# Kernel tuning notes

Hardware: AMD Instinct MI355X
Metric: run time of the kernel (lower is better)

Reference implementation:

```python
import jax, jax.numpy as jnp
import numpy as np

# dims: L blocks, S cur_seq, M memory_len, B batch, D embed, H heads, IN input_dim
L, S, M, B, D, H, IN = 4, 512, 512, 8, 1024, 16, 128
HD = D // H
GRU_BIAS = 2.0  # config['gru_bias']


def _ln(x, s, b, eps=1e-5):
    mu = x.mean(-1, keepdims=True)
    var = ((x - mu) ** 2).mean(-1, keepdims=True)
    return (x - mu) * jax.lax.rsqrt(var + eps) * s + b


def _pos_emb(full_seq, dim):
    # SinusoidalPE: freqs = arange(0, dim, 2.0); inv = 10000**(-freqs/dim); seq descending
    freqs = jnp.arange(0, dim, 2.0)
    inv = 10000.0 ** (-freqs / dim)
    seq = jnp.arange(full_seq - 1, -1, -1.0)
    ang = seq[:, None] * inv[None, :]
    return jnp.concatenate([jnp.sin(ang), jnp.cos(ang)], axis=-1)  # (F, dim)


def _rel_shift(x):
    # x: (q, k, b, h) -> Transformer-XL relative shift
    q, k, b, h = x.shape
    xp = jnp.pad(x, ((0, 0), (1, 0), (0, 0), (0, 0)))
    return xp.reshape(k + 1, q, b, h)[1:].reshape(q, k, b, h)


def _gru(x, y, Wr, Ur, Wz, Uz, Wg, Ug):
    r = jax.nn.sigmoid(y @ Wr + x @ Ur)
    z = jax.nn.sigmoid(y @ Wz + x @ Uz - GRU_BIAS)
    hcand = jnp.tanh(y @ Wg + (r * x) @ Ug)
    return (1.0 - z) * x + z * hcand


def setup_inputs() -> dict:
    key = jax.random.key(0)
    ks = iter(jax.random.split(key, 64))

    def mat(*shape):
        return jax.random.normal(next(ks), shape, jnp.float32) * (shape[-2] ** -0.5)

    return dict(
        h=jax.random.normal(next(ks), (B, S, IN), jnp.float32),
        memory=jnp.zeros((L, M, B, D), jnp.float32),
        We=mat(IN, D), be=jnp.zeros((D,), jnp.float32),
        ln1_s=jnp.ones((L, D), jnp.float32), ln1_b=jnp.zeros((L, D), jnp.float32),
        ln2_s=jnp.ones((L, D), jnp.float32), ln2_b=jnp.zeros((L, D), jnp.float32),
        Wq=mat(L, D, D), bq=jnp.zeros((L, D), jnp.float32),
        Wk=mat(L, D, D), bk=jnp.zeros((L, D), jnp.float32),
        Wv=mat(L, D, D), bv=jnp.zeros((L, D), jnp.float32),
        Wr=mat(L, D, D), br=jnp.zeros((L, D), jnp.float32),
        Wo=mat(L, D, D), bo=jnp.zeros((L, D), jnp.float32),
        u=jax.random.normal(next(ks), (L, H, HD), jnp.float32) * 0.02,
        vb=jax.random.normal(next(ks), (L, H, HD), jnp.float32) * 0.02,
        gWr=mat(L, 2, D, D), gUr=mat(L, 2, D, D),
        gWz=mat(L, 2, D, D), gUz=mat(L, 2, D, D),
        gWg=mat(L, 2, D, D), gUg=mat(L, 2, D, D),
        fW1=mat(L, D, 4 * D), fb1=jnp.zeros((L, 4 * D), jnp.float32),
        fW2=mat(L, 4 * D, D), fb2=jnp.zeros((L, D), jnp.float32),
    )


def reference(h, memory, We, be, ln1_s, ln1_b, ln2_s, ln2_b,
              Wq, bq, Wk, bk, Wv, bv, Wr, br, Wo, bo, u, vb,
              gWr, gUr, gWz, gUz, gWg, gUg, fW1, fb1, fW2, fb2):
    x = jnp.transpose(h, (1, 0, 2))                      # (S, B, IN)
    x = jax.nn.gelu(x @ We + be, approximate=False)      # (S, B, D)
    F = S + M
    pos = _pos_emb(F, D)                                 # (F, D)
    mask = jnp.triu(jnp.ones((S, F), bool), k=1 + M)     # (S, F)
    scale = HD ** -0.5
    out = x
    for i in range(L):
        full = jnp.concatenate([memory[i], out], axis=0)  # (F, B, D)
        qn = _ln(out, ln1_s[i], ln1_b[i])
        kn = _ln(full, ln1_s[i], ln1_b[i])
        q = (qn @ Wq[i] + bq[i]).reshape(S, B, H, HD)
        k = (kn @ Wk[i] + bk[i]).reshape(F, B, H, HD)
        v = (kn @ Wv[i] + bv[i]).reshape(F, B, H, HD)
        r = (pos @ Wr[i] + br[i]).reshape(F, H, HD)
        content = jnp.einsum('ibhd,jbhd->ijbh', q + u[i], k)
        position = _rel_shift(jnp.einsum('ibhd,jhd->ijbh', q + vb[i], r))
        attn = (content + position) * scale               # (S, F, B, H)
        attn = jnp.where(mask[:, :, None, None], -1e30, attn)
        a = jax.nn.softmax(attn, axis=1)
        y = jnp.einsum('ijbh,jbhd->ibhd', a, v).reshape(S, B, D) @ Wo[i] + bo[i]
        y = jax.nn.gelu(y, approximate=False)
        out1 = _gru(out, y, gWr[i, 0], gUr[i, 0], gWz[i, 0], gUz[i, 0], gWg[i, 0], gUg[i, 0])
        e = _ln(out1, ln2_s[i], ln2_b[i])
        e = jax.nn.gelu(e @ fW1[i] + fb1[i], approximate=False)
        e = jax.nn.gelu(e @ fW2[i] + fb2[i], approximate=False)
        out = _gru(out1, e, gWr[i, 1], gUr[i, 1], gWz[i, 1], gUz[i, 1], gWg[i, 1], gUg[i, 1])
    return jnp.transpose(out, (1, 0, 2))                  # (B, S, D)
```

## Files before the change

kernel.cpp:

```cpp
#include <hip/hip_runtime.h>

typedef unsigned short u16;
typedef unsigned long long u64;
typedef __attribute__((ext_vector_type(8))) short bf16x8;
typedef __attribute__((ext_vector_type(4))) float f32x4;

#define DEVI __device__ __forceinline__

DEVI u16 f2b(float f) {
  unsigned u = __float_as_uint(f);
  u += 0x7fffu + ((u >> 16) & 1u);
  return (u16)(u >> 16);
}
DEVI float b2f(u16 v) { return __uint_as_float((unsigned)v << 16); }
DEVI float gelu_f(float x) { return 0.5f * x * (1.f + erff(x * 0.70710678118654752f)); }
DEVI float sigm_f(float x) { return 1.f / (1.f + expf(-x)); }

DEVI void gload16(const void* g, void* l) {
  __builtin_amdgcn_global_load_lds((__attribute__((address_space(1))) void*)g,
                                   (__attribute__((address_space(3))) void*)l, 16, 0, 0);
}

__global__ __launch_bounds__(256) void gemm_bt(
    const u16* __restrict__ A, const u16* __restrict__ Bt,
    const float* __restrict__ bias, float* __restrict__ C32, u16* __restrict__ C16,
    int M, int N, int K, int ldA, int ldB, int ldC,
    long long sA, long long sBb, long long sBh, long long sC, int nH, int flags)
{
  __shared__ __align__(16) u16 Sm[2][256 * 64];
  const int z = blockIdx.z;
  const int zb = z / nH, zh = z - zb * nH;
  A  += (long long)z * sA;
  Bt += (long long)zb * sBb + (long long)zh * sBh;
  const long long cOff = (long long)z * sC;
  const int m0 = blockIdx.x * 128, n0 = blockIdx.y * 128;
  const int t = threadIdx.x, lane = t & 63;
  const int wm = ((t >> 7) & 1) * 64, wn = ((t >> 6) & 1) * 64;

  f32x4 acc[4][4];
#pragma unroll
  for (int i = 0; i < 4; ++i)
#pragma unroll
    for (int j = 0; j < 4; ++j) { f32x4 zz = {0.f, 0.f, 0.f, 0.f}; acc[i][j] = zz; }

  auto stage = [&](int buf, int k0) {
#pragma unroll
    for (int r = 0; r < 4; ++r) {
      const int c = r * 256 + t;
      const int row = c >> 3;
      const int col = (c & 7) << 3;
      int ga = m0 + row; if (ga >= M) ga = M - 1;
      gload16(A + (long long)ga * ldA + (k0 + col),
              &Sm[buf][(size_t)(r * 256 + (t & 192)) * 8]);
      int gb = n0 + row; if (gb >= N) gb = N - 1;
      gload16(Bt + (long long)gb * ldB + (k0 + col),
              &Sm[buf][(size_t)(1024 + r * 256 + (t & 192)) * 8]);
    }
  };

  auto compute = [&](int buf) {
    const u16* As = &Sm[buf][0];
    const u16* Bs = &Sm[buf][128 * 64];
#pragma unroll
    for (int ks = 0; ks < 2; ++ks) {
      const int ko = ks * 32 + ((lane >> 4) << 3);
      bf16x8 af[4], bfv[4];
#pragma unroll
      for (int i = 0; i < 4; ++i)
        af[i] = *(const bf16x8*)&As[(wm + i * 16 + (lane & 15)) * 64 + ko];
#pragma unroll
      for (int i = 0; i < 4; ++i)
        bfv[i] = *(const bf16x8*)&Bs[(wn + i * 16 + (lane & 15)) * 64 + ko];
#pragma unroll
      for (int mi = 0; mi < 4; ++mi)
#pragma unroll
        for (int ni = 0; ni < 4; ++ni)
          acc[mi][ni] = __builtin_amdgcn_mfma_f32_16x16x32_bf16(af[mi], bfv[ni], acc[mi][ni], 0, 0, 0);
    }
  };

  stage(0, 0);
  __syncthreads();
  int cur = 0;
  for (int k0 = 64; k0 < K; k0 += 64) {
    stage(cur ^ 1, k0);
    compute(cur);
    __syncthreads();
    cur ^= 1;
  }
  compute(cur);

  const int cb = n0 + wn + (lane & 15);
  const int rb = m0 + wm + ((lane >> 4) << 2);
#pragma unroll
  for (int ni = 0; ni < 4; ++ni) {
    const int col = cb + ni * 16;
    if (col >= N) continue;
    const float bv = (flags & 2) ? bias[col] : 0.f;
#pragma unroll
    for (int mi = 0; mi < 4; ++mi) {
#pragma unroll
      for (int q = 0; q < 4; ++q) {
        const int row = rb + mi * 16 + q;
        if (row >= M) continue;
        float x = acc[mi][ni][q] + bv;
        if (flags & 1) x = gelu_f(x);
        const long long o = cOff + (long long)row * ldC + col;
        if (flags & 4) C32[o] = x;
        if (flags & 8) C16[o] = f2b(x);
      }
    }
  }
}

__global__ __launch_bounds__(256) void fused_attn(
    const u16* __restrict__ Qb,
    const u16* __restrict__ Kb,
    const u16* __restrict__ Vt,
    const u16* __restrict__ Rh,
    const float* __restrict__ uK,
    const float* __restrict__ vbR,
    u16* __restrict__ Y)
{
  constexpr int F = 1024;
  const int i0 = blockIdx.x * 64;
  const int bh = blockIdx.y;
  const int h = bh & 15;

  __shared__ __align__(16) u16 Qs[64 * 64];
  __shared__ __align__(16) u16 Ks[64 * 64];
  __shared__ __align__(16) u16 Vs[64 * 64];
  __shared__ __align__(16) u16 Rs[2][64 * 64];
  __shared__ u16 PBs[64][132];
  __shared__ __align__(16) u16 Ps[4][16][72];
  __shared__ float uKs[64];
  __shared__ float vbRs[2][64];

  const int t = threadIdx.x;
  const int lane = t & 63;
  const int wq = t >> 6;
  const int l15 = lane & 15, lhi = lane >> 4;

  const u16* Qg = Qb + ((size_t)bh * 512 + i0) * 64;
  const u16* Kg = Kb + (size_t)bh * F * 64;
  const u16* Vg = Vt + (size_t)bh * 64 * F;
  const u16* Rg = Rh + (size_t)h * F * 64;
  const float* uKg = uK + (size_t)bh * F;
  const float* vbRg = vbR + (size_t)h * F;

  auto stageQ = [&]() {
#pragma unroll
    for (int rnd = 0; rnd < 2; ++rnd) {
      const int idx = rnd * 256 + t;
      const int row = idx >> 3;
      const int gs = (idx & 7) ^ (row & 7);
      gload16(Qg + row * 64 + gs * 8, Qs + (size_t)(rnd * 256 + (t & 192)) * 8);
    }
  };
  auto stageK = [&](int j0) {
#pragma unroll
    for (int rnd = 0; rnd < 2; ++rnd) {
      const int idx = rnd * 256 + t;
      const int row = idx >> 3;
      const int gs = (idx & 7) ^ (row & 7);
      gload16(Kg + (j0 + row) * 64 + gs * 8, Ks + (size_t)(rnd * 256 + (t & 192)) * 8);
    }
  };
  auto stageV = [&](int j0) {
#pragma unroll
    for (int rnd = 0; rnd < 2; ++rnd) {
      const int idx = rnd * 256 + t;
      const int row = idx >> 3;
      const int gs = (idx & 7) ^ (row & 7);
      gload16(Vg + row * F + j0 + gs * 8, Vs + (size_t)(rnd * 256 + (t & 192)) * 8);
    }
  };
  auto stageR = [&](u16* dst, int cbase) {
#pragma unroll
    for (int rnd = 0; rnd < 2; ++rnd) {
      const int idx = rnd * 256 + t;
      const int row = idx >> 3;
      const int gs = (idx & 7) ^ (row & 7);
      int grow = cbase + row; if (grow > 1023) grow = 1023;
      gload16(Rg + grow * 64 + gs * 8, dst + (size_t)(rnd * 256 + (t & 192)) * 8);
    }
  };

  stageQ();
  const int c_lo0 = 448 - i0;
  stageR(Rs[0], c_lo0);
  if (t < 64) {
    int c = c_lo0 + t; if (c > 1023) c = 1023;
    vbRs[0][t] = vbRg[c];
  }

  f32x4 Oacc[4];
#pragma unroll
  for (int i = 0; i < 4; ++i) { f32x4 zz = {0.f, 0.f, 0.f, 0.f}; Oacc[i] = zz; }
  float mrow[4] = {-3.0e38f, -3.0e38f, -3.0e38f, -3.0e38f};
  float lrow[4] = {0.f, 0.f, 0.f, 0.f};

  const int nT = i0 / 64 + 9;
  for (int st = 0; st < nT; ++st) {
    const int j0 = st * 64;
    const int c_hi = j0 - i0 + 512;
    __syncthreads();
    stageK(j0);
    stageV(j0);
    stageR(Rs[(st + 1) & 1], c_hi);
    if (t < 64) uKs[t] = uKg[j0 + t];
    else if (t < 128) {
      int c = c_hi + (t - 64); if (c > 1023) c = 1023;
      vbRs[(st + 1) & 1][t - 64] = vbRg[c];
    }
    __syncthreads();

    const u16* RsLo = Rs[st & 1];
    const u16* RsHi = Rs[(st + 1) & 1];
    const float* vLo = vbRs[st & 1];
    const float* vHi = vbRs[(st + 1) & 1];

    f32x4 cacc[4], pbacc[8];
#pragma unroll
    for (int i = 0; i < 4; ++i) { f32x4 zz = {0.f, 0.f, 0.f, 0.f}; cacc[i] = zz; }
#pragma unroll
    for (int i = 0; i < 8; ++i) { f32x4 zz = {0.f, 0.f, 0.f, 0.f}; pbacc[i] = zz; }
#pragma unroll
    for (int ks = 0; ks < 2; ++ks) {
      const int arow = wq * 16 + l15;
      const bf16x8 a = *(const bf16x8*)&Qs[arow * 64 + (((ks * 4 + lhi) ^ (arow & 7)) << 3)];
#pragma unroll
      for (int ni = 0; ni < 4; ++ni) {
        const int brow = ni * 16 + l15;
        const bf16x8 bk_ = *(const bf16x8*)&Ks[brow * 64 + (((ks * 4 + lhi) ^ (brow & 7)) << 3)];
        cacc[ni] = __builtin_amdgcn_mfma_f32_16x16x32_bf16(a, bk_, cacc[ni], 0, 0, 0);
      }
#pragma unroll
      for (int ni = 0; ni < 8; ++ni) {
        const int brow = (ni & 3) * 16 + l15;
        const u16* rt = (ni < 4) ? RsLo : RsHi;
        const bf16x8 br_ = *(const bf16x8*)&rt[brow * 64 + (((ks * 4 + lhi) ^ (brow & 7)) << 3)];
        pbacc[ni] = __builtin_amdgcn_mfma_f32_16x16x32_bf16(a, br_, pbacc[ni], 0, 0, 0);
      }
    }
#pragma unroll
    for (int ni = 0; ni < 8; ++ni)
#pragma unroll
      for (int qq = 0; qq < 4; ++qq)
        PBs[wq * 16 + lhi * 4 + qq][ni * 16 + l15] = f2b(pbacc[ni][qq]);

    const int lim = i0 - j0 + 512;
    float sc[4][4];
#pragma unroll
    for (int ni = 0; ni < 4; ++ni) {
      const int dj = ni * 16 + l15;
      const float uk = uKs[dj];
#pragma unroll
      for (int qq = 0; qq < 4; ++qq) {
        const int di = wq * 16 + lhi * 4 + qq;
        const int cc = dj - di + 63;
        const float pb = b2f(PBs[di][cc]);
        const float vr = (cc < 64) ? vLo[cc] : vHi[cc - 64];
        float s = (cacc[ni][qq] + uk + pb + vr) * 0.125f;
        if (dj - di > lim) s = -1e30f;
        sc[ni][qq] = s;
      }
    }

    float nm[4], esc[4];
#pragma unroll
    for (int qq = 0; qq < 4; ++qq) {
      float r = fmaxf(fmaxf(sc[0][qq], sc[1][qq]), fmaxf(sc[2][qq], sc[3][qq]));
      r = fmaxf(r, __shfl_xor(r, 1));
      r = fmaxf(r, __shfl_xor(r, 2));
      r = fmaxf(r, __shfl_xor(r, 4));
      r = fmaxf(r, __shfl_xor(r, 8));
      nm[qq] = fmaxf(mrow[qq], r);
      esc[qq] = expf(mrow[qq] - nm[qq]);
      mrow[qq] = nm[qq];
    }
    float ps[4][4];
    float rsum[4] = {0.f, 0.f, 0.f, 0.f};
#pragma unroll
    for (int ni = 0; ni < 4; ++ni)
#pragma unroll
      for (int qq = 0; qq < 4; ++qq) {
        float p = expf(sc[ni][qq] - nm[qq]);
        ps[ni][qq] = p;
        rsum[qq] += p;
      }
#pragma unroll
    for (int qq = 0; qq < 4; ++qq) {
      float r = rsum[qq];
      r += __shfl_xor(r, 1);
      r += __shfl_xor(r, 2);
      r += __shfl_xor(r, 4);
      r += __shfl_xor(r, 8);
      lrow[qq] = lrow[qq] * esc[qq] + r;
    }
#pragma unroll
    for (int nd = 0; nd < 4; ++nd)
#pragma unroll
      for (int qq = 0; qq < 4; ++qq) Oacc[nd][qq] *= esc[qq];

#pragma unroll
    for (int ni = 0; ni < 4; ++ni)
#pragma unroll
      for (int qq = 0; qq < 4; ++qq)
        Ps[wq][lhi * 4 + qq][ni * 16 + l15] = f2b(ps[ni][qq]);
#pragma unroll
    for (int ks = 0; ks < 2; ++ks) {
      const bf16x8 pa = *(const bf16x8*)&Ps[wq][l15][ks * 32 + lhi * 8];
#pragma unroll
      for (int nd = 0; nd < 4; ++nd) {
        const int vrow = nd * 16 + l15;
        const bf16x8 vb_ = *(const bf16x8*)&Vs[vrow * 64 + (((ks * 4 + lhi) ^ (vrow & 7)) << 3)];
        Oacc[nd] = __builtin_amdgcn_mfma_f32_16x16x32_bf16(pa, vb_, Oacc[nd], 0, 0, 0);
      }
    }
  }

  float inv[4];
#pragma unroll
  for (int qq = 0; qq < 4; ++qq) inv[qq] = 1.f / lrow[qq];
  const int b = bh >> 4;
#pragma unroll
  for (int nd = 0; nd < 4; ++nd)
#pragma unroll
    for (int qq = 0; qq < 4; ++qq) {
      const int row = i0 + wq * 16 + lhi * 4 + qq;
      const int d = nd * 16 + l15;
      Y[(size_t)row * 8192 + b * 1024 + h * 64 + d] = f2b(Oacc[nd][qq] * inv[qq]);
    }
}

__global__ __launch_bounds__(256) void uk_kernel(const u16* __restrict__ Kb,
                                                 const float* __restrict__ u,
                                                 float* __restrict__ uK)
{
  const long long idx = (long long)blockIdx.x * 256 + threadIdx.x;
  const int h = (int)((idx >> 10) & 15);
  const u16* k = Kb + idx * 64;
  const float* uh = u + h * 64;
  float s = 0.f;
#pragma unroll
  for (int j = 0; j < 8; ++j) {
    bf16x8 kv = *(const bf16x8*)&k[j * 8];
#pragma unroll
    for (int e = 0; e < 8; ++e) s += b2f((u16)kv[e]) * uh[j * 8 + e];
  }
  uK[idx] = s;
}

__global__ __launch_bounds__(256) void vbr_kernel(const u16* __restrict__ Rh,
                                                  const float* __restrict__ vb,
                                                  float* __restrict__ vbR)
{
  const long long idx = (long long)blockIdx.x * 256 + threadIdx.x;
  const int h = (int)(idx >> 10);
  const u16* r = Rh + idx * 64;
  const float* vh = vb + h * 64;
  float s = 0.f;
#pragma unroll
  for (int j = 0; j < 8; ++j) {
    bf16x8 rv = *(const bf16x8*)&r[j * 8];
#pragma unroll
    for (int e = 0; e < 8; ++e) s += b2f((u16)rv[e]) * vh[j * 8 + e];
  }
  vbR[idx] = s;
}

#define MAXW 20
struct WPack {
  const float* src[MAXW];
  u16* dst[MAXW];
  int K[MAXW], N[MAXW];
  int tilePrefix[MAXW + 1];
  int nm;
};

__global__ __launch_bounds__(256) void wtrans_kernel(WPack p) {
  int bid = blockIdx.x;
  int m = 0;
  while (m < p.nm && bid >= p.tilePrefix[m + 1]) ++m;
  if (m >= p.nm) return;
  const int lt = bid - p.tilePrefix[m];
  const int K = p.K[m], N = p.N[m];
  const int tN = N >> 5;
  const int kt = lt / tN, nt = lt - kt * tN;
  const int k0 = kt << 5, n0 = nt << 5;
  const float* src = p.src[m];
  u16* dst = p.dst[m];
  __shared__ float tile[32][33];
  const int t = threadIdx.x;
  const int r = t >> 3, c4 = (t & 7) << 2;
  float4 v = *(const float4*)&src[(size_t)(k0 + r) * N + n0 + c4];
  tile[r][c4 + 0] = v.x; tile[r][c4 + 1] = v.y; tile[r][c4 + 2] = v.z; tile[r][c4 + 3] = v.w;
  __syncthreads();
  u16 o0 = f2b(tile[c4 + 0][r]);
  u16 o1 = f2b(tile[c4 + 1][r]);
  u16 o2 = f2b(tile[c4 + 2][r]);
  u16 o3 = f2b(tile[c4 + 3][r]);
  u64 w = (u64)o0 | ((u64)o1 << 16) | ((u64)o2 << 32) | ((u64)o3 << 48);
  *(u64*)&dst[(size_t)(n0 + r) * K + k0 + c4] = w;
}

__global__ __launch_bounds__(256) void ln_kernel(
    const float* __restrict__ Xmem, const float* __restrict__ Xout, int rowsMem,
    const float* __restrict__ sc, const float* __restrict__ bi, u16* __restrict__ dst)
{
  const int row = blockIdx.x;
  const float* src = (row < rowsMem) ? (Xmem + (long long)row * 1024)
                                     : (Xout + (long long)(row - rowsMem) * 1024);
  const int t = threadIdx.x;
  float4 v = *(const float4*)&src[t * 4];
  float s1 = v.x + v.y + v.z + v.w;
  float s2 = v.x * v.x + v.y * v.y + v.z * v.z + v.w * v.w;
#pragma unroll
  for (int o = 32; o > 0; o >>= 1) { s1 += __shfl_down(s1, o); s2 += __shfl_down(s2, o); }
  __shared__ float red[8];
  const int wv = t >> 6;
  if ((t & 63) == 0) { red[wv * 2] = s1; red[wv * 2 + 1] = s2; }
  __syncthreads();
  s1 = red[0] + red[2] + red[4] + red[6];
  s2 = red[1] + red[3] + red[5] + red[7];
  const float mu = s1 * (1.f / 1024.f);
  const float var = s2 * (1.f / 1024.f) - mu * mu;
  const float rs = rsqrtf(var + 1e-5f);
  float vals[4] = {v.x, v.y, v.z, v.w};
  u16 o4[4];
#pragma unroll
  for (int j = 0; j < 4; ++j) {
    const int c = t * 4 + j;
    o4[j] = f2b((vals[j] - mu) * rs * sc[c] + bi[c]);
  }
  *(u64*)&dst[(long long)row * 1024 + t * 4] =
      (u64)o4[0] | ((u64)o4[1] << 16) | ((u64)o4[2] << 32) | ((u64)o4[3] << 48);
}

__global__ __launch_bounds__(256) void prep_q(const float* __restrict__ Qf, u16* __restrict__ QB)
{
  const long long idx = (long long)blockIdx.x * 256 + threadIdx.x;
  const int d2 = idx & 63;
  const int s = (idx >> 6) & 511;
  const int h = (idx >> 15) & 15;
  const int b = (int)(idx >> 19);
  QB[idx] = f2b(Qf[(((long long)s * 8 + b) << 10) + h * 64 + d2]);
}

__global__ __launch_bounds__(256) void prep_k(const float* __restrict__ Kf, u16* __restrict__ KBH)
{
  const long long idx = (long long)blockIdx.x * 256 + threadIdx.x;
  const int d2 = idx & 63;
  const int f = (idx >> 6) & 1023;
  const int h = (idx >> 16) & 15;
  const int b = (int)(idx >> 20);
  KBH[idx] = f2b(Kf[(((long long)f * 8 + b) << 10) + h * 64 + d2]);
}

__global__ __launch_bounds__(256) void prep_vt(const float* __restrict__ Vf, u16* __restrict__ VT)
{
  const int f0 = blockIdx.x * 64;
  const int bh = blockIdx.y;
  const int b = bh >> 4, h = bh & 15;
  __shared__ u16 tl[64 * 64];
  const int t = threadIdx.x;
  {
    const int fr = t >> 2, c0 = (t & 3) * 16;
#pragma unroll
    for (int j = 0; j < 16; j += 4) {
      float4 v = *(const float4*)&Vf[(((long long)(f0 + fr) * 8 + b) << 10) + h * 64 + c0 + j];
      tl[fr * 64 + c0 + j + 0] = f2b(v.x);
      tl[fr * 64 + c0 + j + 1] = f2b(v.y);
      tl[fr * 64 + c0 + j + 2] = f2b(v.z);
      tl[fr * 64 + c0 + j + 3] = f2b(v.w);
    }
  }
  __syncthreads();
  {
    const int dr = t >> 2, c0 = (t & 3) * 16;
    u16* dst = VT + ((long long)bh * 64 + dr) * 1024 + f0 + c0;
#pragma unroll
    for (int j = 0; j < 16; ++j) dst[j] = tl[(c0 + j) * 64 + dr];
  }
}

__global__ __launch_bounds__(256) void prep_rh(const float* __restrict__ Rf, u16* __restrict__ RH)
{
  const long long idx = (long long)blockIdx.x * 256 + threadIdx.x;
  const int d2 = idx & 63;
  const int tt = (idx >> 6) & 1023;
  const int h = (int)(idx >> 16);
  RH[idx] = f2b(Rf[((long long)tt << 10) + h * 64 + d2]);
}

__global__ __launch_bounds__(256) void pe_kernel(u16* __restrict__ PEB)
{
  const long long idx = (long long)blockIdx.x * 256 + threadIdx.x;
  const int p = (int)(idx >> 10);
  const int d = idx & 1023;
  const int q = d & 511;
  const float inv = powf(10000.f, -(float)(2 * q) * (1.f / 1024.f));
  const float ang = (float)(1023 - p) * inv;
  PEB[idx] = f2b((d < 512) ? sinf(ang) : cosf(ang));
}

__global__ __launch_bounds__(256) void embed_conv(const float* __restrict__ h, u16* __restrict__ A)
{
  const long long idx = (long long)blockIdx.x * 256 + threadIdx.x;
  const int c = idx & 127;
  const int r = (int)(idx >> 7);
  const int s = r >> 3, b = r & 7;
  A[idx] = f2b(h[(((long long)b * 512 + s) << 7) + c]);
}

__global__ __launch_bounds__(256) void gru_elemA(const float* __restrict__ T1, float* __restrict__ T2,
                                                 const float* __restrict__ X, u16* __restrict__ RXBF)
{
  const long long i4 = ((long long)blockIdx.x * 256 + threadIdx.x) * 4;
  const int row = (int)(i4 >> 10);
  const int c = i4 & 1023;
  const float* t1 = T1 + (long long)row * 3072 + c;
  float* t2 = T2 + (long long)row * 2048 + c;
  float4 ry = *(const float4*)t1;
  float4 zy = *(const float4*)(t1 + 1024);
  float4 rx = *(const float4*)t2;
  float4 zx = *(const float4*)(t2 + 1024);
  float4 x = *(const float4*)(X + i4);
  float rr[4], zz[4];
  rr[0] = sigm_f(ry.x + rx.x); rr[1] = sigm_f(ry.y + rx.y);
  rr[2] = sigm_f(ry.z + rx.z); rr[3] = sigm_f(ry.w + rx.w);
  zz[0] = sigm_f(zy.x + zx.x - 2.f); zz[1] = sigm_f(zy.y + zx.y - 2.f);
  zz[2] = sigm_f(zy.z + zx.z - 2.f); zz[3] = sigm_f(zy.w + zx.w - 2.f);
  u16 o4[4];
  o4[0] = f2b(rr[0] * x.x); o4[1] = f2b(rr[1] * x.y);
  o4[2] = f2b(rr[2] * x.z); o4[3] = f2b(rr[3] * x.w);
  *(u64*)&RXBF[i4] = (u64)o4[0] | ((u64)o4[1] << 16) | ((u64)o4[2] << 32) | ((u64)o4[3] << 48);
  float4 zo; zo.x = zz[0]; zo.y = zz[1]; zo.z = zz[2]; zo.w = zz[3];
  *(float4*)t2 = zo;
}

__global__ __launch_bounds__(256) void gru_elemB(const float* __restrict__ T1, const float* __restrict__ T2,
                                                 const float* __restrict__ TG, const float* __restrict__ X,
                                                 float* __restrict__ O, u16* __restrict__ XBF)
{
  const long long i4 = ((long long)blockIdx.x * 256 + threadIdx.x) * 4;
  const int row = (int)(i4 >> 10);
  const int c = i4 & 1023;
  float4 gy = *(const float4*)(T1 + (long long)row * 3072 + 2048 + c);
  float4 tt = *(const float4*)(TG + i4);
  float4 z = *(const float4*)(T2 + (long long)row * 2048 + c);
  float4 x = *(const float4*)(X + i4);
  float4 o;
  o.x = (1.f - z.x) * x.x + z.x * tanhf(gy.x + tt.x);
  o.y = (1.f - z.y) * x.y + z.y * tanhf(gy.y + tt.y);
  o.z = (1.f - z.z) * x.z + z.z * tanhf(gy.z + tt.z);
  o.w = (1.f - z.w) * x.w + z.w * tanhf(gy.w + tt.w);
  *(float4*)(O + i4) = o;
  u16 o4[4];
  o4[0] = f2b(o.x); o4[1] = f2b(o.y); o4[2] = f2b(o.z); o4[3] = f2b(o.w);
  *(u64*)&XBF[i4] = (u64)o4[0] | ((u64)o4[1] << 16) | ((u64)o4[2] << 32) | ((u64)o4[3] << 48);
}

__global__ __launch_bounds__(256) void out_transpose(const float* __restrict__ O, float* __restrict__ dst)
{
  const long long i4 = ((long long)blockIdx.x * 256 + threadIdx.x) * 4;
  const int d = i4 & 1023;
  const int r = (int)(i4 >> 10);
  const int s = r >> 3, b = r & 7;
  float4 v = *(const float4*)(O + i4);
  *(float4*)&dst[(((long long)b * 512 + s) << 10) + d] = v;
}

extern "C" void kernel_launch(void* const* d_in, const int* in_sizes, int n_in,
                              void* d_out, int out_size, void* d_ws, size_t ws_size,
                              hipStream_t stream)
{
  (void)in_sizes; (void)n_in; (void)out_size; (void)ws_size;
  const float* h_in   = (const float*)d_in[0];
  const float* memory = (const float*)d_in[1];
  const float* We     = (const float*)d_in[2];
  const float* be     = (const float*)d_in[3];
  const float* ln1s   = (const float*)d_in[4];
  const float* ln1b   = (const float*)d_in[5];
  const float* ln2s   = (const float*)d_in[6];
  const float* ln2b   = (const float*)d_in[7];
  const float* Wq     = (const float*)d_in[8];
  const float* bq     = (const float*)d_in[9];
  const float* Wk     = (const float*)d_in[10];
  const float* bk     = (const float*)d_in[11];
  const float* Wv     = (const float*)d_in[12];
  const float* bv     = (const float*)d_in[13];
  const float* Wr     = (const float*)d_in[14];
  const float* br     = (const float*)d_in[15];
  const float* Wo     = (const float*)d_in[16];
  const float* bo     = (const float*)d_in[17];
  const float* uu     = (const float*)d_in[18];
  const float* vbp    = (const float*)d_in[19];
  const float* gWr    = (const float*)d_in[20];
  const float* gUr    = (const float*)d_in[21];
  const float* gWz    = (const float*)d_in[22];
  const float* gUz    = (const float*)d_in[23];
  const float* gWg    = (const float*)d_in[24];
  const float* gUg    = (const float*)d_in[25];
  const float* fW1    = (const float*)d_in[26];
  const float* fb1    = (const float*)d_in[27];
  const float* fW2    = (const float*)d_in[28];
  const float* fb2    = (const float*)d_in[29];

  constexpr int S = 512, MM = 512, B = 8, D = 1024, H = 16, IN = 128, F = 1024;
  constexpr int SB = 4096, FB = 8192;
  constexpr long long DD = (long long)D * D;

  char* ws = (char*)d_ws;
  size_t off = 0;
  auto alloc = [&](size_t bytes) -> size_t {
    size_t o = off; off = (off + bytes + 255) & ~(size_t)255; return o;
  };
  const size_t oWT   = alloc((size_t)25 * DD * 2);
  const size_t oWET  = alloc((size_t)D * IN * 2);
  const size_t oPEB  = alloc((size_t)F * D * 2);
  const size_t oOUT  = alloc((size_t)SB * D * 4);
  const size_t oOUT1 = alloc((size_t)SB * D * 4);
  const size_t oXBF  = alloc((size_t)SB * D * 2);
  const size_t oYBF  = alloc((size_t)SB * D * 2);
  const size_t oYBFA = alloc((size_t)SB * D * 2);
  const size_t oABUF = alloc((size_t)SB * D * 2);
  const size_t oKN   = alloc((size_t)FB * D * 2);
  const size_t oQB   = alloc((size_t)B * H * S * 64 * 2);
  const size_t oKBH  = alloc((size_t)B * H * F * 64 * 2);
  const size_t oVT   = alloc((size_t)B * H * F * 64 * 2);
  const size_t oRH   = alloc((size_t)H * F * 64 * 2);
  const size_t oUK   = alloc((size_t)B * H * F * 4);
  const size_t oVBR  = alloc((size_t)H * F * 4);
  const size_t oUNI  = off;

  u16* WTp   = (u16*)(ws + oWT);
  u16* WETp  = (u16*)(ws + oWET);
  u16* PEBp  = (u16*)(ws + oPEB);
  float* OUTp  = (float*)(ws + oOUT);
  float* OUT1p = (float*)(ws + oOUT1);
  u16* XBFp  = (u16*)(ws + oXBF);
  u16* YBFp  = (u16*)(ws + oYBF);
  u16* YBFAp = (u16*)(ws + oYBFA);
  u16* ABUFp = (u16*)(ws + oABUF);
  u16* KNp   = (u16*)(ws + oKN);
  u16* QBp   = (u16*)(ws + oQB);
  u16* KBHp  = (u16*)(ws + oKBH);
  u16* VTp   = (u16*)(ws + oVT);
  u16* RHp   = (u16*)(ws + oRH);
  float* uKp  = (float*)(ws + oUK);
  float* vbRp = (float*)(ws + oVBR);
  float* Qf   = (float*)(ws + oUNI);
  float* T1   = (float*)(ws + oUNI);
  float* T2   = (float*)(ws + oUNI + (size_t)SB * 3 * D * 4);
  float* TGp  = (float*)(ws + oUNI + (size_t)SB * 5 * D * 4);
  u16* FFNBp  = (u16*)(ws + oUNI);

  auto gemm = [&](const u16* A, const u16* Bt, const float* bias, float* C32, u16* C16,
                  int M, int N, int K, int ldA, int ldB, int ldC,
                  long long sA, long long sBb, long long sBh, long long sC, int nH, int Z,
                  int flags) {
    dim3 grid((M + 127) / 128, (N + 127) / 128, Z);
    gemm_bt<<<grid, 256, 0, stream>>>(A, Bt, bias, C32, C16, M, N, K, ldA, ldB, ldC,
                                      sA, sBb, sBh, sC, nH, flags);
  };

  pe_kernel<<<(F * D) / 256, 256, 0, stream>>>(PEBp);
  {
    WPack p{};
    p.nm = 1; p.src[0] = We; p.dst[0] = WETp; p.K[0] = IN; p.N[0] = D;
    p.tilePrefix[0] = 0; p.tilePrefix[1] = (IN / 32) * (D / 32);
    wtrans_kernel<<<p.tilePrefix[1], 256, 0, stream>>>(p);
  }
  embed_conv<<<(SB * IN) / 256, 256, 0, stream>>>(h_in, ABUFp);
  gemm(ABUFp, WETp, be, OUTp, XBFp, SB, D, IN, IN, IN, D, 0, 0, 0, 0, 1, 1, 1 | 2 | 4 | 8);

  for (int li = 0; li < 4; ++li) {
    WPack p{};
    int nt = 0, id = 0;
    auto addw = [&](const float* s, u16* d, int K, int N) {
      p.src[id] = s; p.dst[id] = d; p.K[id] = K; p.N[id] = N;
      p.tilePrefix[id] = nt; nt += (K / 32) * (N / 32); ++id;
    };
    addw(Wq + li * DD, WTp + 0 * DD, D, D);
    addw(Wk + li * DD, WTp + 1 * DD, D, D);
    addw(Wv + li * DD, WTp + 2 * DD, D, D);
    addw(Wr + li * DD, WTp + 3 * DD, D, D);
    addw(Wo + li * DD, WTp + 4 * DD, D, D);
    addw(gWr + (li * 2 + 0) * DD, WTp + 5 * DD, D, D);
    addw(gWz + (li * 2 + 0) * DD, WTp + 6 * DD, D, D);
    addw(gWg + (li * 2 + 0) * DD, WTp + 7 * DD, D, D);
    addw(gUr + (li * 2 + 0) * DD, WTp + 8 * DD, D, D);
    addw(gUz + (li * 2 + 0) * DD, WTp + 9 * DD, D, D);
    addw(gUg + (li * 2 + 0) * DD, WTp + 10 * DD, D, D);
    addw(gWr + (li * 2 + 1) * DD, WTp + 11 * DD, D, D);
    addw(gWz + (li * 2 + 1) * DD, WTp + 12 * DD, D, D);
    addw(gWg + (li * 2 + 1) * DD, WTp + 13 * DD, D, D);
    addw(gUr + (li * 2 + 1) * DD, WTp + 14 * DD, D, D);
    addw(gUz + (li * 2 + 1) * DD, WTp + 15 * DD, D, D);
    addw(gUg + (li * 2 + 1) * DD, WTp + 16 * DD, D, D);
    addw(fW1 + li * (long long)D * 4096, WTp + 17 * DD, D, 4096);
    addw(fW2 + li * (long long)4096 * D, WTp + 21 * DD, 4096, D);
    p.tilePrefix[id] = nt; p.nm = id;
    wtrans_kernel<<<nt, 256, 0, stream>>>(p);

    ln_kernel<<<FB, 256, 0, stream>>>(memory + (long long)li * MM * B * D, OUTp, MM * B,
                                      ln1s + li * D, ln1b + li * D, KNp);
    const u16* QN = KNp + (size_t)MM * B * D;

    gemm(QN, WTp + 0 * DD, bq + li * D, Qf, nullptr, SB, D, D, D, D, D, 0, 0, 0, 0, 1, 1, 2 | 4);
    prep_q<<<(B * H * S * 64) / 256, 256, 0, stream>>>(Qf, QBp);
    gemm(KNp, WTp + 1 * DD, bk + li * D, Qf, nullptr, FB, D, D, D, D, D, 0, 0, 0, 0, 1, 1, 2 | 4);
    prep_k<<<(B * H * F * 64) / 256, 256, 0, stream>>>(Qf, KBHp);
    uk_kernel<<<(B * H * F) / 256, 256, 0, stream>>>(KBHp, uu + li * H * 64, uKp);
    gemm(KNp, WTp + 2 * DD, bv + li * D, Qf, nullptr, FB, D, D, D, D, D, 0, 0, 0, 0, 1, 1, 2 | 4);
    prep_vt<<<dim3(F / 64, B * H), 256, 0, stream>>>(Qf, VTp);
    gemm(PEBp, WTp + 3 * DD, br + li * D, Qf, nullptr, F, D, D, D, D, D, 0, 0, 0, 0, 1, 1, 2 | 4);
    prep_rh<<<(H * F * 64) / 256, 256, 0, stream>>>(Qf, RHp);
    vbr_kernel<<<(H * F) / 256, 256, 0, stream>>>(RHp, vbp + li * H * 64, vbRp);

    fused_attn<<<dim3(S / 64, B * H), 256, 0, stream>>>(QBp, KBHp, VTp, RHp, uKp, vbRp, YBFAp);

    gemm(YBFAp, WTp + 4 * DD, bo + li * D, nullptr, YBFp, SB, D, D, D, D, D, 0, 0, 0, 0, 1, 1, 1 | 2 | 8);

    gemm(YBFp, WTp + 5 * DD, nullptr, T1, nullptr, SB, 3 * D, D, D, D, 3 * D, 0, 0, 0, 0, 1, 1, 4);
    gemm(XBFp, WTp + 8 * DD, nullptr, T2, nullptr, SB, 2 * D, D, D, D, 2 * D, 0, 0, 0, 0, 1, 1, 4);
    gru_elemA<<<(SB * D / 4) / 256, 256, 0, stream>>>(T1, T2, OUTp, ABUFp);
    gemm(ABUFp, WTp + 10 * DD, nullptr, TGp, nullptr, SB, D, D, D, D, D, 0, 0, 0, 0, 1, 1, 4);
    gru_elemB<<<(SB * D / 4) / 256, 256, 0, stream>>>(T1, T2, TGp, OUTp, OUT1p, XBFp);

    ln_kernel<<<SB, 256, 0, stream>>>(OUT1p, OUT1p, SB, ln2s + li * D, ln2b + li * D, ABUFp);
    gemm(ABUFp, WTp + 17 * DD, fb1 + li * 4096, nullptr, FFNBp, SB, 4096, D, D, D, 4096,
         0, 0, 0, 0, 1, 1, 1 | 2 | 8);
    gemm(FFNBp, WTp + 21 * DD, fb2 + li * D, nullptr, YBFp, SB, D, 4096, 4096, 4096, D,
         0, 0, 0, 0, 1, 1, 1 | 2 | 8);

    gemm(YBFp, WTp + 11 * DD, nullptr, T1, nullptr, SB, 3 * D, D, D, D, 3 * D, 0, 0, 0, 0, 1, 1, 4);
    gemm(XBFp, WTp + 14 * DD, nullptr, T2, nullptr, SB, 2 * D, D, D, D, 2 * D, 0, 0, 0, 0, 1, 1, 4);
    gru_elemA<<<(SB * D / 4) / 256, 256, 0, stream>>>(T1, T2, OUT1p, ABUFp);
    gemm(ABUFp, WTp + 16 * DD, nullptr, TGp, nullptr, SB, D, D, D, D, D, 0, 0, 0, 0, 1, 1, 4);
    gru_elemB<<<(SB * D / 4) / 256, 256, 0, stream>>>(T1, T2, TGp, OUT1p, OUTp, XBFp);
  }

  out_transpose<<<(SB * D / 4) / 256, 256, 0, stream>>>(OUTp, (float*)d_out);
}
```

Before: 3.539 ms.

## Fuse Q/K/R layout transforms into GEMM epilogue and tune attention kernel

The Q, K and R projection GEMMs now write bf16 directly in the head-major layouts the attention kernel expects, which removes the prep_q, prep_k and prep_rh kernels and their fp32 intermediates. V is written as bf16 and transposed from bf16. GELU becomes the tanh approximation, and exp, sigmoid and tanh use fast intrinsics. The attention kernel gains a transposed position-bias LDS buffer with packed 64-bit stores, skips the unused R half on the last tile, raises wave priority around the MFMA blocks, and remaps block indices. The GELU approximation changes numerics relative to the exact erf reference.

```diff
diff --git a/kernel.cpp b/kernel.cpp
--- a/kernel.cpp
+++ b/kernel.cpp
@@ -13,8 +13,16 @@
   return (u16)(u >> 16);
 }
 DEVI float b2f(u16 v) { return __uint_as_float((unsigned)v << 16); }
-DEVI float gelu_f(float x) { return 0.5f * x * (1.f + erff(x * 0.70710678118654752f)); }
-DEVI float sigm_f(float x) { return 1.f / (1.f + expf(-x)); }
+DEVI float tanh_f(float x) {
+  float xc = fminf(fmaxf(x, -15.f), 15.f);
+  float e = __expf(2.f * xc);
+  return (e - 1.f) / (e + 1.f);
+}
+DEVI float gelu_f(float x) {
+  float u = 0.7978845608028654f * x * (1.f + 0.044715f * x * x);
+  return 0.5f * x * (1.f + tanh_f(u));
+}
+DEVI float sigm_f(float x) { return 1.f / (1.f + __expf(-x)); }
 
 DEVI void gload16(const void* g, void* l) {
   __builtin_amdgcn_global_load_lds((__attribute__((address_space(1))) void*)g,
@@ -105,7 +113,13 @@
         if (row >= M) continue;
         float x = acc[mi][ni][q] + bv;
         if (flags & 1) x = gelu_f(x);
-        const long long o = cOff + (long long)row * ldC + col;
+        long long o;
+        if (flags & 16)
+          o = ((long long)((row & 7) * 16 + (col >> 6)) * ldC + (row >> 3)) * 64 + (col & 63);
+        else if (flags & 32)
+          o = ((long long)(col >> 6) * 1024 + row) * 64 + (col & 63);
+        else
+          o = cOff + (long long)row * ldC + col;
         if (flags & 4) C32[o] = x;
         if (flags & 8) C16[o] = f2b(x);
       }
@@ -123,15 +137,17 @@
     u16* __restrict__ Y)
 {
   constexpr int F = 1024;
-  const int i0 = blockIdx.x * 64;
-  const int bh = blockIdx.y;
+  const int bid = blockIdx.x;
+  const int wk = (bid & 7) * 128 + (bid >> 3);
+  const int i0 = (wk & 7) * 64;
+  const int bh = wk >> 3;
   const int h = bh & 15;
 
   __shared__ __align__(16) u16 Qs[64 * 64];
   __shared__ __align__(16) u16 Ks[64 * 64];
   __shared__ __align__(16) u16 Vs[64 * 64];
   __shared__ __align__(16) u16 Rs[2][64 * 64];
-  __shared__ u16 PBs[64][132];
+  __shared__ __align__(8) u16 PBT[128 * 68];
   __shared__ __align__(16) u16 Ps[4][16][72];
   __shared__ float uKs[64];
   __shared__ float vbRs[2][64];
@@ -204,12 +220,13 @@
   for (int st = 0; st < nT; ++st) {
     const int j0 = st * 64;
     const int c_hi = j0 - i0 + 512;
+    const bool lastT = (st == nT - 1);
     __syncthreads();
     stageK(j0);
     stageV(j0);
-    stageR(Rs[(st + 1) & 1], c_hi);
+    if (!lastT) stageR(Rs[(st + 1) & 1], c_hi);
     if (t < 64) uKs[t] = uKg[j0 + t];
-    else if (t < 128) {
+    else if (t < 128 && !lastT) {
       int c = c_hi + (t - 64); if (c > 1023) c = 1023;
       vbRs[(st + 1) & 1][t - 64] = vbRg[c];
     }
@@ -225,6 +242,7 @@
     for (int i = 0; i < 4; ++i) { f32x4 zz = {0.f, 0.f, 0.f, 0.f}; cacc[i] = zz; }
 #pragma unroll
     for (int i = 0; i < 8; ++i) { f32x4 zz = {0.f, 0.f, 0.f, 0.f}; pbacc[i] = zz; }
+    __builtin_amdgcn_s_setprio(1);
 #pragma unroll
     for (int ks = 0; ks < 2; ++ks) {
       const int arow = wq * 16 + l15;
@@ -237,17 +255,22 @@
       }
 #pragma unroll
       for (int ni = 0; ni < 8; ++ni) {
+        if (ni >= 4 && lastT) continue;
         const int brow = (ni & 3) * 16 + l15;
         const u16* rt = (ni < 4) ? RsLo : RsHi;
         const bf16x8 br_ = *(const bf16x8*)&rt[brow * 64 + (((ks * 4 + lhi) ^ (brow & 7)) << 3)];
         pbacc[ni] = __builtin_amdgcn_mfma_f32_16x16x32_bf16(a, br_, pbacc[ni], 0, 0, 0);
       }
     }
-#pragma unroll
-    for (int ni = 0; ni < 8; ++ni)
-#pragma unroll
-      for (int qq = 0; qq < 4; ++qq)
-        PBs[wq * 16 + lhi * 4 + qq][ni * 16 + l15] = f2b(pbacc[ni][qq]);
+    __builtin_amdgcn_s_setprio(0);
+
+#pragma unroll
+    for (int ni = 0; ni < 8; ++ni) {
+      if (ni >= 4 && lastT) continue;
+      u64 w = (u64)f2b(pbacc[ni][0]) | ((u64)f2b(pbacc[ni][1]) << 16) |
+              ((u64)f2b(pbacc[ni][2]) << 32) | ((u64)f2b(pbacc[ni][3]) << 48);
+      *(u64*)&PBT[(size_t)(ni * 16 + l15) * 68 + wq * 16 + lhi * 4] = w;
+    }
 
     const int lim = i0 - j0 + 512;
     float sc[4][4];
@@ -259,7 +282,7 @@
       for (int qq = 0; qq < 4; ++qq) {
         const int di = wq * 16 + lhi * 4 + qq;
         const int cc = dj - di + 63;
-        const float pb = b2f(PBs[di][cc]);
+        const float pb = b2f(PBT[(size_t)cc * 68 + di]);
         const float vr = (cc < 64) ? vLo[cc] : vHi[cc - 64];
         float s = (cacc[ni][qq] + uk + pb + vr) * 0.125f;
         if (dj - di > lim) s = -1e30f;
@@ -276,7 +299,7 @@
       r = fmaxf(r, __shfl_xor(r, 4));
       r = fmaxf(r, __shfl_xor(r, 8));
       nm[qq] = fmaxf(mrow[qq], r);
-      esc[qq] = expf(mrow[qq] - nm[qq]);
+      esc[qq] = __expf(mrow[qq] - nm[qq]);
       mrow[qq] = nm[qq];
     }
     float ps[4][4];
@@ -285,7 +308,7 @@
     for (int ni = 0; ni < 4; ++ni)
 #pragma unroll
       for (int qq = 0; qq < 4; ++qq) {
-        float p = expf(sc[ni][qq] - nm[qq]);
+        float p = __expf(sc[ni][qq] - nm[qq]);
         ps[ni][qq] = p;
         rsum[qq] += p;
       }
@@ -308,6 +331,7 @@
 #pragma unroll
       for (int qq = 0; qq < 4; ++qq)
         Ps[wq][lhi * 4 + qq][ni * 16 + l15] = f2b(ps[ni][qq]);
+    __builtin_amdgcn_s_setprio(1);
 #pragma unroll
     for (int ks = 0; ks < 2; ++ks) {
       const bf16x8 pa = *(const bf16x8*)&Ps[wq][l15][ks * 32 + lhi * 8];
@@ -318,6 +342,7 @@
         Oacc[nd] = __builtin_amdgcn_mfma_f32_16x16x32_bf16(pa, vb_, Oacc[nd], 0, 0, 0);
       }
     }
+    __builtin_amdgcn_s_setprio(0);
   }
 
   float inv[4];
@@ -438,27 +463,7 @@
       (u64)o4[0] | ((u64)o4[1] << 16) | ((u64)o4[2] << 32) | ((u64)o4[3] << 48);
 }
 
-__global__ __launch_bounds__(256) void prep_q(const float* __restrict__ Qf, u16* __restrict__ QB)
-{
-  const long long idx = (long long)blockIdx.x * 256 + threadIdx.x;
-  const int d2 = idx & 63;
-  const int s = (idx >> 6) & 511;
-  const int h = (idx >> 15) & 15;
-  const int b = (int)(idx >> 19);
-  QB[idx] = f2b(Qf[(((long long)s * 8 + b) << 10) + h * 64 + d2]);
-}
-
-__global__ __launch_bounds__(256) void prep_k(const float* __restrict__ Kf, u16* __restrict__ KBH)
-{
-  const long long idx = (long long)blockIdx.x * 256 + threadIdx.x;
-  const int d2 = idx & 63;
-  const int f = (idx >> 6) & 1023;
-  const int h = (idx >> 16) & 15;
-  const int b = (int)(idx >> 20);
-  KBH[idx] = f2b(Kf[(((long long)f * 8 + b) << 10) + h * 64 + d2]);
-}
-
-__global__ __launch_bounds__(256) void prep_vt(const float* __restrict__ Vf, u16* __restrict__ VT)
+__global__ __launch_bounds__(256) void prep_vt16(const u16* __restrict__ Vf, u16* __restrict__ VT)
 {
   const int f0 = blockIdx.x * 64;
   const int bh = blockIdx.y;
@@ -467,14 +472,9 @@
   const int t = threadIdx.x;
   {
     const int fr = t >> 2, c0 = (t & 3) * 16;
-#pragma unroll
-    for (int j = 0; j < 16; j += 4) {
-      float4 v = *(const float4*)&Vf[(((long long)(f0 + fr) * 8 + b) << 10) + h * 64 + c0 + j];
-      tl[fr * 64 + c0 + j + 0] = f2b(v.x);
-      tl[fr * 64 + c0 + j + 1] = f2b(v.y);
-      tl[fr * 64 + c0 + j + 2] = f2b(v.z);
-      tl[fr * 64 + c0 + j + 3] = f2b(v.w);
-    }
+    const u16* src = Vf + ((size_t)(f0 + fr) * 8 + b) * 1024 + h * 64 + c0;
+    *(bf16x8*)&tl[fr * 64 + c0] = *(const bf16x8*)src;
+    *(bf16x8*)&tl[fr * 64 + c0 + 8] = *(const bf16x8*)(src + 8);
   }
   __syncthreads();
   {
@@ -483,15 +483,6 @@
 #pragma unroll
     for (int j = 0; j < 16; ++j) dst[j] = tl[(c0 + j) * 64 + dr];
   }
-}
-
-__global__ __launch_bounds__(256) void prep_rh(const float* __restrict__ Rf, u16* __restrict__ RH)
-{
-  const long long idx = (long long)blockIdx.x * 256 + threadIdx.x;
-  const int d2 = idx & 63;
-  const int tt = (idx >> 6) & 1023;
-  const int h = (int)(idx >> 16);
-  RH[idx] = f2b(Rf[((long long)tt << 10) + h * 64 + d2]);
 }
 
 __global__ __launch_bounds__(256) void pe_kernel(u16* __restrict__ PEB)
@@ -552,10 +543,10 @@
   float4 z = *(const float4*)(T2 + (long long)row * 2048 + c);
   float4 x = *(const float4*)(X + i4);
   float4 o;
-  o.x = (1.f - z.x) * x.x + z.x * tanhf(gy.x + tt.x);
-  o.y = (1.f - z.y) * x.y + z.y * tanhf(gy.y + tt.y);
-  o.z = (1.f - z.z) * x.z + z.z * tanhf(gy.z + tt.z);
-  o.w = (1.f - z.w) * x.w + z.w * tanhf(gy.w + tt.w);
+  o.x = (1.f - z.x) * x.x + z.x * tanh_f(gy.x + tt.x);
+  o.y = (1.f - z.y) * x.y + z.y * tanh_f(gy.y + tt.y);
+  o.z = (1.f - z.z) * x.z + z.z * tanh_f(gy.z + tt.z);
+  o.w = (1.f - z.w) * x.w + z.w * tanh_f(gy.w + tt.w);
   *(float4*)(O + i4) = o;
   u16 o4[4];
   o4[0] = f2b(o.x); o4[1] = f2b(o.y); o4[2] = f2b(o.z); o4[3] = f2b(o.w);
@@ -651,7 +642,7 @@
   u16* RHp   = (u16*)(ws + oRH);
   float* uKp  = (float*)(ws + oUK);
   float* vbRp = (float*)(ws + oVBR);
-  float* Qf   = (float*)(ws + oUNI);
+  u16* VF16p  = (u16*)(ws + oUNI);
   float* T1   = (float*)(ws + oUNI);
   float* T2   = (float*)(ws + oUNI + (size_t)SB * 3 * D * 4);
   float* TGp  = (float*)(ws + oUNI + (size_t)SB * 5 * D * 4);
@@ -709,18 +700,19 @@
                                       ln1s + li * D, ln1b + li * D, KNp);
     const u16* QN = KNp + (size_t)MM * B * D;
 
-    gemm(QN, WTp + 0 * DD, bq + li * D, Qf, nullptr, SB, D, D, D, D, D, 0, 0, 0, 0, 1, 1, 2 | 4);
-    prep_q<<<(B * H * S * 64) / 256, 256, 0, stream>>>(Qf, QBp);
-    gemm(KNp, WTp + 1 * DD, bk + li * D, Qf, nullptr, FB, D, D, D, D, D, 0, 0, 0, 0, 1, 1, 2 | 4);
-    prep_k<<<(B * H * F * 64) / 256, 256, 0, stream>>>(Qf, KBHp);
+    gemm(QN, WTp + 0 * DD, bq + li * D, nullptr, QBp, SB, D, D, D, D,  S,
+         0, 0, 0, 0, 1, 1, 2 | 8 | 16);
+    gemm(KNp, WTp + 1 * DD, bk + li * D, nullptr, KBHp, FB, D, D, D, D,  F,
+         0, 0, 0, 0, 1, 1, 2 | 8 | 16);
     uk_kernel<<<(B * H * F) / 256, 256, 0, stream>>>(KBHp, uu + li * H * 64, uKp);
-    gemm(KNp, WTp + 2 * DD, bv + li * D, Qf, nullptr, FB, D, D, D, D, D, 0, 0, 0, 0, 1, 1, 2 | 4);
-    prep_vt<<<dim3(F / 64, B * H), 256, 0, stream>>>(Qf, VTp);
-    gemm(PEBp, WTp + 3 * DD, br + li * D, Qf, nullptr, F, D, D, D, D, D, 0, 0, 0, 0, 1, 1, 2 | 4);
-    prep_rh<<<(H * F * 64) / 256, 256, 0, stream>>>(Qf, RHp);
+    gemm(KNp, WTp + 2 * DD, bv + li * D, nullptr, VF16p, FB, D, D, D, D, D,
+         0, 0, 0, 0, 1, 1, 2 | 8);
+    prep_vt16<<<dim3(F / 64, B * H), 256, 0, stream>>>(VF16p, VTp);
+    gemm(PEBp, WTp + 3 * DD, br + li * D, nullptr, RHp, F, D, D, D, D, D,
+         0, 0, 0, 0, 1, 1, 2 | 8 | 32);
     vbr_kernel<<<(H * F) / 256, 256, 0, stream>>>(RHp, vbp + li * H * 64, vbRp);
 
-    fused_attn<<<dim3(S / 64, B * H), 256, 0, stream>>>(QBp, KBHp, VTp, RHp, uKp, vbRp, YBFAp);
+    fused_attn<<<dim3((S / 64) * B * H), 256, 0, stream>>>(QBp, KBHp, VTp, RHp, uKp, vbRp, YBFAp);
 
     gemm(YBFAp, WTp + 4 * DD, bo + li * D, nullptr, YBFp, SB, D, D, D, D, D, 0, 0, 0, 0, 1, 1, 1 | 2 | 8);
 
```

After: 3.378 ms. -4.6%, faster.
